# Performance work log

Hardware: AMD Instinct MI355X
Metric: run time of the kernel (lower is better)

Reference implementation:

```python
import jax, jax.numpy as jnp
import numpy as np

B, N, T, H = 16, 256, 96, 128
EPS = 1e-5


def setup_inputs() -> dict:
    key = jax.random.key(0)
    ks = jax.random.split(key, 9)
    return {
        "x": jax.random.normal(ks[0], (B, N, T), dtype=jnp.float32),
        "Wp": jax.random.normal(ks[1], (T, H), dtype=jnp.float32) / np.sqrt(T),
        "bp": jax.random.normal(ks[2], (H,), dtype=jnp.float32) * 0.01,
        "Wf": jax.random.normal(ks[3], (3 * H, H), dtype=jnp.float32) / np.sqrt(3 * H),
        "bf": jax.random.normal(ks[4], (H,), dtype=jnp.float32) * 0.01,
        "gamma": jnp.ones((H,), dtype=jnp.float32),
        "beta": jnp.zeros((H,), dtype=jnp.float32),
        "node_emb": jax.random.normal(ks[5], (N, H), dtype=jnp.float32),
        "time_emb": jax.random.normal(ks[6], (T, H), dtype=jnp.float32),
    }


def reference(x, Wp, bp, Wf, bf, gamma, beta, node_emb, time_emb):
    # input projection: [B,N,T] @ [T,H] -> [B,N,H]
    proj = jnp.einsum("bnt,th->bnh", x, Wp) + bp
    # Decompose the Linear over the concat [proj | node_pos | time_pos]:
    # cat(...) @ Wf == proj@W1 + node@W2 + time@W3  (same math, no huge concat)
    W1, W2, W3 = Wf[:H], Wf[H:2 * H], Wf[2 * H:]
    pre = (jnp.einsum("bnh,hk->bnk", proj, W1)[:, :, None, :]      # [B,N,1,H]
           + jnp.einsum("nh,hk->nk", node_emb, W2)[None, :, None, :]  # [1,N,1,H]
           + jnp.einsum("th,hk->tk", time_emb, W3)[None, None, :, :]  # [1,1,T,H]
           + bf)
    h = jax.nn.relu(pre)  # [B,N,T,H]
    mean = jnp.mean(h, axis=-1, keepdims=True)
    var = jnp.mean(jnp.square(h - mean), axis=-1, keepdims=True)
    return (h - mean) * jax.lax.rsqrt(var + EPS) * gamma + beta
```

## Files before the change

### kernel.cpp

```cpp
#include <hip/hip_runtime.h>
#include <hip/hip_bf16.h>

#define Bn 16
#define Nn 256
#define Tn 96
#define Hn 128
#define EPSf 1e-5f

__global__ __launch_bounds__(128) void precompute_kernel(
    const float* __restrict__ Wp, const float* __restrict__ bp,
    const float* __restrict__ Wf, const float* __restrict__ bf,
    const float* __restrict__ node_emb, const float* __restrict__ time_emb,
    float* __restrict__ M, float* __restrict__ E, float* __restrict__ Ct) {
  __shared__ float row[Hn];
  const int k = threadIdx.x;
  const int bid = blockIdx.x;
  if (bid < Tn) {
    const int t = bid;
    row[k] = Wp[t * Hn + k];
    __syncthreads();
    float acc = 0.f;
#pragma unroll 8
    for (int h = 0; h < Hn; ++h) acc = fmaf(row[h], Wf[h * Hn + k], acc);
    M[t * Hn + k] = acc;
  } else if (bid < Tn + Nn) {
    const int n = bid - Tn;
    row[k] = node_emb[n * Hn + k];
    __syncthreads();
    float acc = 0.f;
#pragma unroll 8
    for (int h = 0; h < Hn; ++h) acc = fmaf(row[h], Wf[(Hn + h) * Hn + k], acc);
    __syncthreads();
    row[k] = bp[k];
    __syncthreads();
#pragma unroll 8
    for (int h = 0; h < Hn; ++h) acc = fmaf(row[h], Wf[h * Hn + k], acc);
    E[n * Hn + k] = acc;
  } else {
    const int t = bid - Tn - Nn;
    row[k] = time_emb[t * Hn + k];
    __syncthreads();
    float acc = bf[k];
#pragma unroll 8
    for (int h = 0; h < Hn; ++h) acc = fmaf(row[h], Wf[(2 * Hn + h) * Hn + k], acc);
    Ct[t * Hn + k] = acc;
  }
}

__device__ __forceinline__ float swz_xor1(float v) {
  return __int_as_float(__builtin_amdgcn_ds_swizzle(__float_as_int(v), 0x041F));
}
__device__ __forceinline__ float swz_xor2(float v) {
  return __int_as_float(__builtin_amdgcn_ds_swizzle(__float_as_int(v), 0x081F));
}
__device__ __forceinline__ float swz_xor4(float v) {
  return __int_as_float(__builtin_amdgcn_ds_swizzle(__float_as_int(v), 0x101F));
}
__device__ __forceinline__ float swz_xor8(float v) {
  return __int_as_float(__builtin_amdgcn_ds_swizzle(__float_as_int(v), 0x201F));
}

__global__ __launch_bounds__(256) void main_kernel(
    const float* __restrict__ x, const float* __restrict__ M,
    const float* __restrict__ E, const float* __restrict__ Ct,
    const float* __restrict__ gamma, const float* __restrict__ beta,
    float* __restrict__ out) {
  const int bn = blockIdx.x;
  const int n = bn & (Nn - 1);
  __shared__ float xs[Tn];
  __shared__ __align__(16) float as[Hn];
  const int tid = threadIdx.x;

  if (tid < Tn) xs[tid] = x[bn * Tn + tid];
  __syncthreads();
  if (tid < Hn) {
    float acc = E[n * Hn + tid];
#pragma unroll 8
    for (int t = 0; t < Tn; ++t) acc = fmaf(xs[t], M[t * Hn + tid], acc);
    as[tid] = acc;
  }
  __syncthreads();

  const int wave = tid >> 6;
  const int lane = tid & 63;
  const int r  = lane >> 4;
  const int cg = lane & 15;
  const int cb = cg * 8;

  const float4 a0 = *(const float4*)&as[cb];
  const float4 a1 = *(const float4*)&as[cb + 4];
  const float4 g0 = *(const float4*)&gamma[cb];
  const float4 g1 = *(const float4*)&gamma[cb + 4];
  const float4 q0 = *(const float4*)&beta[cb];
  const float4 q1 = *(const float4*)&beta[cb + 4];
  const float inv128 = 1.f / 128.f;

#pragma unroll
  for (int i = 0; i < Tn / 16; ++i) {
    const int t = i * 16 + wave * 4 + r;
    const float4 c0 = *(const float4*)&Ct[t * Hn + cb];
    const float4 c1 = *(const float4*)&Ct[t * Hn + cb + 4];
    const float h0 = fmaxf(a0.x + c0.x, 0.f);
    const float h1 = fmaxf(a0.y + c0.y, 0.f);
    const float h2 = fmaxf(a0.z + c0.z, 0.f);
    const float h3 = fmaxf(a0.w + c0.w, 0.f);
    const float h4 = fmaxf(a1.x + c1.x, 0.f);
    const float h5 = fmaxf(a1.y + c1.y, 0.f);
    const float h6 = fmaxf(a1.z + c1.z, 0.f);
    const float h7 = fmaxf(a1.w + c1.w, 0.f);

    float s = ((h0 + h1) + (h2 + h3)) + ((h4 + h5) + (h6 + h7));
    float ss = h0 * h0;
    ss = fmaf(h1, h1, ss); ss = fmaf(h2, h2, ss); ss = fmaf(h3, h3, ss);
    ss = fmaf(h4, h4, ss); ss = fmaf(h5, h5, ss); ss = fmaf(h6, h6, ss);
    ss = fmaf(h7, h7, ss);

    s += swz_xor1(s);  ss += swz_xor1(ss);
    s += swz_xor2(s);  ss += swz_xor2(ss);
    s += swz_xor4(s);  ss += swz_xor4(ss);
    s += swz_xor8(s);  ss += swz_xor8(ss);

    const float mean = s * inv128;
    const float var  = fmaf(-mean, mean, ss * inv128);
    const float inv  = rsqrtf(var + EPSf);

    float4 o0, o1;
    o0.x = fmaf((h0 - mean) * inv, g0.x, q0.x);
    o0.y = fmaf((h1 - mean) * inv, g0.y, q0.y);
    o0.z = fmaf((h2 - mean) * inv, g0.z, q0.z);
    o0.w = fmaf((h3 - mean) * inv, g0.w, q0.w);
    o1.x = fmaf((h4 - mean) * inv, g1.x, q1.x);
    o1.y = fmaf((h5 - mean) * inv, g1.y, q1.y);
    o1.z = fmaf((h6 - mean) * inv, g1.z, q1.z);
    o1.w = fmaf((h7 - mean) * inv, g1.w, q1.w);

    float* op = &out[((size_t)bn * Tn + t) * Hn + cb];
    *(float4*)op = o0;
    *(float4*)(op + 4) = o1;
  }
}

extern "C" void kernel_launch(void* const* d_in, const int* in_sizes, int n_in,
                              void* d_out, int out_size, void* d_ws, size_t ws_size,
                              hipStream_t stream) {
  const float* x        = (const float*)d_in[0];
  const float* Wp       = (const float*)d_in[1];
  const float* bp       = (const float*)d_in[2];
  const float* Wf       = (const float*)d_in[3];
  const float* bf       = (const float*)d_in[4];
  const float* gamma    = (const float*)d_in[5];
  const float* beta     = (const float*)d_in[6];
  const float* node_emb = (const float*)d_in[7];
  const float* time_emb = (const float*)d_in[8];
  float* out = (float*)d_out;

  float* ws = (float*)d_ws;
  float* M  = ws;
  float* E  = ws + Tn * Hn;
  float* Ct = ws + Tn * Hn + Nn * Hn;

  precompute_kernel<<<Tn + Nn + Tn, 128, 0, stream>>>(Wp, bp, Wf, bf, node_emb,
                                                      time_emb, M, E, Ct);
  main_kernel<<<Bn * Nn, 256, 0, stream>>>(x, M, E, Ct, gamma, beta, out);
}
```

Before: 232.6 us.

## Split projection into separate kernel, use DPP reductions and nontemporal stores

Moves the per-(b,n) projection GEMV into its own kernel that writes A to workspace, so the streaming LayerNorm kernel no longer has a serialized GEMV prologue and block-level syncs before its output writes. The cross-lane reduction switches from ds_swizzle to DPP row operations, and output stores become nontemporal to avoid polluting the cache with the large output. The split adds an extra kernel launch and a workspace round trip for A, and it falls back to the fused kernel when the workspace is too small.

Result: slower. 291.9 us (+25.5%).

```diff
diff --git a/kernel.cpp b/kernel.cpp
--- a/kernel.cpp
+++ b/kernel.cpp
@@ -1,11 +1,12 @@
 #include <hip/hip_runtime.h>
-#include <hip/hip_bf16.h>
 
 #define Bn 16
 #define Nn 256
 #define Tn 96
 #define Hn 128
 #define EPSf 1e-5f
+
+typedef float v4f __attribute__((ext_vector_type(4)));
 
 __global__ __launch_bounds__(128) void precompute_kernel(
     const float* __restrict__ Wp, const float* __restrict__ bp,
@@ -47,20 +48,114 @@
   }
 }
 
-__device__ __forceinline__ float swz_xor1(float v) {
-  return __int_as_float(__builtin_amdgcn_ds_swizzle(__float_as_int(v), 0x041F));
-}
-__device__ __forceinline__ float swz_xor2(float v) {
-  return __int_as_float(__builtin_amdgcn_ds_swizzle(__float_as_int(v), 0x081F));
-}
-__device__ __forceinline__ float swz_xor4(float v) {
-  return __int_as_float(__builtin_amdgcn_ds_swizzle(__float_as_int(v), 0x101F));
-}
-__device__ __forceinline__ float swz_xor8(float v) {
-  return __int_as_float(__builtin_amdgcn_ds_swizzle(__float_as_int(v), 0x201F));
-}
-
-__global__ __launch_bounds__(256) void main_kernel(
+__global__ __launch_bounds__(256) void proj_kernel(
+    const float* __restrict__ x, const float* __restrict__ M,
+    const float* __restrict__ E, float* __restrict__ A) {
+  __shared__ float xs[2][Tn];
+  const int tid = threadIdx.x;
+  const int row0 = blockIdx.x * 2;
+  if (tid < 2 * Tn) {
+    const int rr = tid >= Tn;
+    xs[rr][tid - rr * Tn] = x[row0 * Tn + tid];
+  }
+  __syncthreads();
+  const int half = tid >> 7;
+  const int k = tid & 127;
+  const int bn = row0 + half;
+  const int n = bn & (Nn - 1);
+  float acc = E[n * Hn + k];
+#pragma unroll 8
+  for (int t = 0; t < Tn; ++t) acc = fmaf(xs[half][t], M[t * Hn + k], acc);
+  A[bn * Hn + k] = acc;
+}
+
+template <int CTRL>
+__device__ __forceinline__ float dpp_add(float v) {
+  return v + __int_as_float(__builtin_amdgcn_update_dpp(
+                 0, __float_as_int(v), CTRL, 0xF, 0xF, true));
+}
+__device__ __forceinline__ float row16_sum(float v) {
+  v = dpp_add<0xB1>(v);
+  v = dpp_add<0x4E>(v);
+  v = dpp_add<0x124>(v);
+  v = dpp_add<0x128>(v);
+  return v;
+}
+
+__device__ __forceinline__ void ln_row_store(
+    const float4 a0, const float4 a1, const float4 g0, const float4 g1,
+    const float4 q0, const float4 q1, const float* __restrict__ ct_row,
+    float* __restrict__ op) {
+  const float4 c0 = *(const float4*)ct_row;
+  const float4 c1 = *(const float4*)(ct_row + 4);
+  const float h0 = fmaxf(a0.x + c0.x, 0.f);
+  const float h1 = fmaxf(a0.y + c0.y, 0.f);
+  const float h2 = fmaxf(a0.z + c0.z, 0.f);
+  const float h3 = fmaxf(a0.w + c0.w, 0.f);
+  const float h4 = fmaxf(a1.x + c1.x, 0.f);
+  const float h5 = fmaxf(a1.y + c1.y, 0.f);
+  const float h6 = fmaxf(a1.z + c1.z, 0.f);
+  const float h7 = fmaxf(a1.w + c1.w, 0.f);
+
+  float s = ((h0 + h1) + (h2 + h3)) + ((h4 + h5) + (h6 + h7));
+  float ss = h0 * h0;
+  ss = fmaf(h1, h1, ss); ss = fmaf(h2, h2, ss); ss = fmaf(h3, h3, ss);
+  ss = fmaf(h4, h4, ss); ss = fmaf(h5, h5, ss); ss = fmaf(h6, h6, ss);
+  ss = fmaf(h7, h7, ss);
+
+  s = row16_sum(s);
+  ss = row16_sum(ss);
+
+  const float inv128 = 1.f / 128.f;
+  const float mean = s * inv128;
+  const float var = fmaf(-mean, mean, ss * inv128);
+  const float inv = rsqrtf(var + EPSf);
+
+  v4f o0, o1;
+  o0.x = fmaf((h0 - mean) * inv, g0.x, q0.x);
+  o0.y = fmaf((h1 - mean) * inv, g0.y, q0.y);
+  o0.z = fmaf((h2 - mean) * inv, g0.z, q0.z);
+  o0.w = fmaf((h3 - mean) * inv, g0.w, q0.w);
+  o1.x = fmaf((h4 - mean) * inv, g1.x, q1.x);
+  o1.y = fmaf((h5 - mean) * inv, g1.y, q1.y);
+  o1.z = fmaf((h6 - mean) * inv, g1.z, q1.z);
+  o1.w = fmaf((h7 - mean) * inv, g1.w, q1.w);
+
+  __builtin_nontemporal_store(o0, (v4f*)op);
+  __builtin_nontemporal_store(o1, (v4f*)(op + 4));
+}
+
+__global__ __launch_bounds__(256) void stream_kernel(
+    const float* __restrict__ A, const float* __restrict__ Ct,
+    const float* __restrict__ gamma, const float* __restrict__ beta,
+    float* __restrict__ out) {
+  const int bn = blockIdx.x;
+  const int tid = threadIdx.x;
+  const int wave = tid >> 6;
+  const int lane = tid & 63;
+  const int r = lane >> 4;
+  const int cg = lane & 15;
+  const int cb = cg * 8;
+
+  const float4 a0 = *(const float4*)&A[bn * Hn + cb];
+  const float4 a1 = *(const float4*)&A[bn * Hn + cb + 4];
+  const float4 g0 = *(const float4*)&gamma[cb];
+  const float4 g1 = *(const float4*)&gamma[cb + 4];
+  const float4 q0 = *(const float4*)&beta[cb];
+  const float4 q1 = *(const float4*)&beta[cb + 4];
+
+  const int tbase = wave * 4 + r;
+  float* outb = out + (size_t)bn * Tn * Hn + cb;
+  const float* ctb = Ct + cb;
+
+#pragma unroll
+  for (int i = 0; i < Tn / 16; ++i) {
+    const int t = i * 16 + tbase;
+    ln_row_store(a0, a1, g0, g1, q0, q1, ctb + t * Hn, outb + (size_t)t * Hn);
+  }
+}
+
+__global__ __launch_bounds__(256) void fused_kernel(
     const float* __restrict__ x, const float* __restrict__ M,
     const float* __restrict__ E, const float* __restrict__ Ct,
     const float* __restrict__ gamma, const float* __restrict__ beta,
@@ -83,7 +178,7 @@
 
   const int wave = tid >> 6;
   const int lane = tid & 63;
-  const int r  = lane >> 4;
+  const int r = lane >> 4;
   const int cg = lane & 15;
   const int cb = cg * 8;
 
@@ -93,50 +188,15 @@
   const float4 g1 = *(const float4*)&gamma[cb + 4];
   const float4 q0 = *(const float4*)&beta[cb];
   const float4 q1 = *(const float4*)&beta[cb + 4];
-  const float inv128 = 1.f / 128.f;
+
+  const int tbase = wave * 4 + r;
+  float* outb = out + (size_t)bn * Tn * Hn + cb;
+  const float* ctb = Ct + cb;
 
 #pragma unroll
   for (int i = 0; i < Tn / 16; ++i) {
-    const int t = i * 16 + wave * 4 + r;
-    const float4 c0 = *(const float4*)&Ct[t * Hn + cb];
-    const float4 c1 = *(const float4*)&Ct[t * Hn + cb + 4];
-    const float h0 = fmaxf(a0.x + c0.x, 0.f);
-    const float h1 = fmaxf(a0.y + c0.y, 0.f);
-    const float h2 = fmaxf(a0.z + c0.z, 0.f);
-    const float h3 = fmaxf(a0.w + c0.w, 0.f);
-    const float h4 = fmaxf(a1.x + c1.x, 0.f);
-    const float h5 = fmaxf(a1.y + c1.y, 0.f);
-    const float h6 = fmaxf(a1.z + c1.z, 0.f);
-    const float h7 = fmaxf(a1.w + c1.w, 0.f);
-
-    float s = ((h0 + h1) + (h2 + h3)) + ((h4 + h5) + (h6 + h7));
-    float ss = h0 * h0;
-    ss = fmaf(h1, h1, ss); ss = fmaf(h2, h2, ss); ss = fmaf(h3, h3, ss);
-    ss = fmaf(h4, h4, ss); ss = fmaf(h5, h5, ss); ss = fmaf(h6, h6, ss);
-    ss = fmaf(h7, h7, ss);
-
-    s += swz_xor1(s);  ss += swz_xor1(ss);
-    s += swz_xor2(s);  ss += swz_xor2(ss);
-    s += swz_xor4(s);  ss += swz_xor4(ss);
-    s += swz_xor8(s);  ss += swz_xor8(ss);
-
-    const float mean = s * inv128;
-    const float var  = fmaf(-mean, mean, ss * inv128);
-    const float inv  = rsqrtf(var + EPSf);
-
-    float4 o0, o1;
-    o0.x = fmaf((h0 - mean) * inv, g0.x, q0.x);
-    o0.y = fmaf((h1 - mean) * inv, g0.y, q0.y);
-    o0.z = fmaf((h2 - mean) * inv, g0.z, q0.z);
-    o0.w = fmaf((h3 - mean) * inv, g0.w, q0.w);
-    o1.x = fmaf((h4 - mean) * inv, g1.x, q1.x);
-    o1.y = fmaf((h5 - mean) * inv, g1.y, q1.y);
-    o1.z = fmaf((h6 - mean) * inv, g1.z, q1.z);
-    o1.w = fmaf((h7 - mean) * inv, g1.w, q1.w);
-
-    float* op = &out[((size_t)bn * Tn + t) * Hn + cb];
-    *(float4*)op = o0;
-    *(float4*)(op + 4) = o1;
+    const int t = i * 16 + tbase;
+    ln_row_store(a0, a1, g0, g1, q0, q1, ctb + t * Hn, outb + (size_t)t * Hn);
   }
 }
 
@@ -158,8 +218,17 @@
   float* M  = ws;
   float* E  = ws + Tn * Hn;
   float* Ct = ws + Tn * Hn + Nn * Hn;
+  float* A  = ws + Tn * Hn + Nn * Hn + Tn * Hn;
+
+  const size_t need =
+      (size_t)(Tn * Hn + Nn * Hn + Tn * Hn + Bn * Nn * Hn) * sizeof(float);
 
   precompute_kernel<<<Tn + Nn + Tn, 128, 0, stream>>>(Wp, bp, Wf, bf, node_emb,
                                                       time_emb, M, E, Ct);
-  main_kernel<<<Bn * Nn, 256, 0, stream>>>(x, M, E, Ct, gamma, beta, out);
-}
+  if (ws_size >= need) {
+    proj_kernel<<<Bn * Nn / 2, 256, 0, stream>>>(x, M, E, A);
+    stream_kernel<<<Bn * Nn, 256, 0, stream>>>(A, Ct, gamma, beta, out);
+  } else {
+    fused_kernel<<<Bn * Nn, 256, 0, stream>>>(x, M, E, Ct, gamma, beta, out);
+  }
+}
```
